# Optimization experiments

Measured on AMD Instinct MI355X. Metric: run time of the kernel, lower is better.

Reference implementation:

```python
import jax, jax.numpy as jnp
import numpy as np

D = 1024  # input_size
H = 1024  # hidden_size
B = 128
R = 512


def _lin(x, W, b):
    return x @ W + b


def setup_inputs() -> dict:
    key = jax.random.key(0)
    ks = jax.random.split(key, 20)
    s = 0.02
    inp = {
        "V": jax.random.normal(ks[0], (B, R, D), jnp.float32),
        "s_t": jax.random.normal(ks[1], (B, D), jnp.float32),
        "h_t": jax.random.normal(ks[2], (B, D), jnp.float32),
        # weights stored [in, out] (y = x @ W + b)
        "Wv": jax.random.normal(ks[3], (D, H), jnp.float32) * s,
        "bv": jnp.zeros((H,), jnp.float32),
        "Wsp": jax.random.normal(ks[4], (D, D), jnp.float32) * s,
        "bsp": jnp.zeros((D,), jnp.float32),
        "Wsa": jax.random.normal(ks[5], (D, H), jnp.float32) * s,
        "bsa": jnp.zeros((H,), jnp.float32),
        "Whp": jax.random.normal(ks[6], (D, D), jnp.float32) * s,
        "bhp": jnp.zeros((D,), jnp.float32),
        "Wha": jax.random.normal(ks[7], (D, H), jnp.float32) * s,
        "bha": jnp.zeros((H,), jnp.float32),
        "Wal": jax.random.normal(ks[8], (H, 1), jnp.float32) * s,
        "bal": jnp.zeros((1,), jnp.float32),
        "Wcp": jax.random.normal(ks[9], (D, D), jnp.float32) * s,
        "bcp": jnp.zeros((D,), jnp.float32),
    }
    return inp


def reference(V, s_t, h_t, Wv, bv, Wsp, bsp, Wsa, bsa, Whp, bhp, Wha, bha, Wal, bal, Wcp, bcp):
    v_embed = jax.nn.relu(_lin(V, Wv, bv))           # [B,R,H]
    s_proj = jax.nn.relu(_lin(s_t, Wsp, bsp))        # [B,D]
    s_att = _lin(s_proj, Wsa, bsa)                   # [B,H]
    h_proj = jnp.tanh(_lin(h_t, Whp, bhp))           # [B,D]
    h_att = _lin(h_proj, Wha, bha)                   # [B,H]
    regions = jnp.concatenate([V, s_proj[:, None, :]], axis=1)           # [B,R+1,D]
    regions_att = jnp.concatenate([v_embed, s_att[:, None, :]], axis=1)  # [B,R+1,H]
    alpha_input = jnp.tanh(regions_att + h_att[:, None, :])              # [B,R+1,H]
    scores = (_lin(alpha_input, Wal, bal)).squeeze(-1)                   # [B,R+1]
    alpha = jax.nn.softmax(scores, axis=1)                               # [B,R+1]
    context = jnp.einsum("br,brd->bd", alpha, regions)                   # [B,D]
    z_t = jnp.tanh(_lin(context + h_proj, Wcp, bcp))                     # [B,D]
    return z_t
```

## Files before the change

### kernel.cpp

```cpp
#include <hip/hip_runtime.h>


typedef __bf16 bf16x8 __attribute__((ext_vector_type(8)));
typedef float floatx4 __attribute__((ext_vector_type(4)));

__device__ __forceinline__ float tanh_fast(float x) {
    x = fminf(10.0f, fmaxf(-10.0f, x));
    float e = exp2f(x * 2.885390081777927f);
    return (e - 1.0f) * __builtin_amdgcn_rcpf(e + 1.0f);
}

__global__ __launch_bounds__(256) void wvt_kernel(
    const float* __restrict__ Wv, __bf16* __restrict__ WvT) {
    __shared__ float tile[64][65];
    const int k0 = blockIdx.x * 64, n0 = blockIdx.y * 64;
    const int c = threadIdx.x & 63, r = threadIdx.x >> 6;
#pragma unroll
    for (int i = 0; i < 16; ++i)
        tile[r + i * 4][c] = Wv[(size_t)(k0 + r + i * 4) * 1024 + n0 + c];
    __syncthreads();
#pragma unroll
    for (int i = 0; i < 16; ++i)
        WvT[(size_t)(n0 + r + i * 4) * 1024 + k0 + c] =
            (__bf16)tile[c][r + i * 4];
}

__global__ __launch_bounds__(512) void small_gemm_k(
    const float* __restrict__ A0, const float* __restrict__ W0,
    const float* __restrict__ b0, float* __restrict__ C0, int act0,
    const float* __restrict__ A1, const float* __restrict__ W1,
    const float* __restrict__ b1, float* __restrict__ C1, int act1) {
    const float* A; const float* W; const float* bs; float* C; int act;
    if (blockIdx.z == 0) { A = A0; W = W0; bs = b0; C = C0; act = act0; }
    else                 { A = A1; W = W1; bs = b1; C = C1; act = act1; }
    __shared__ float red[3][8][128];
    const int tid = threadIdx.x;
    const int nl = tid & 127, kq = tid >> 7;
    const int n = blockIdx.x * 128 + nl;
    const int m0 = blockIdx.y * 8;
    const float* Ab = A + m0 * 1024;
    float acc[8] = {};
    const int kbeg = kq * 256, kend = kbeg + 256;
#pragma unroll 4
    for (int k = kbeg; k < kend; ++k) {
        float w = W[(size_t)k * 1024 + n];
#pragma unroll
        for (int mi = 0; mi < 8; ++mi)
            acc[mi] = fmaf(Ab[mi * 1024 + k], w, acc[mi]);
    }
    if (kq > 0) {
#pragma unroll
        for (int mi = 0; mi < 8; ++mi) red[kq - 1][mi][nl] = acc[mi];
    }
    __syncthreads();
    if (kq == 0) {
        float bias = bs[n];
#pragma unroll
        for (int mi = 0; mi < 8; ++mi) {
            float v = acc[mi] + red[0][mi][nl] + red[1][mi][nl] +
                      red[2][mi][nl] + bias;
            if (act == 1) v = fmaxf(v, 0.0f);
            else if (act == 2) v = tanh_fast(v);
            C[(size_t)(m0 + mi) * 1024 + n] = v;
        }
    }
}

__global__ __launch_bounds__(256, 3) void score_gemm_k(
    const float* __restrict__ V, const __bf16* __restrict__ WvT,
    const float* __restrict__ bv, const float* __restrict__ h_att,
    const float* __restrict__ Wal, float* __restrict__ scores) {
    __shared__ __bf16 As[2][128 * 40];
    __shared__ __bf16 Bs[2][128 * 32];

    const int tid = threadIdx.x;
    const int bid = blockIdx.x;
    const int xcd = bid & 7;
    const int j = bid >> 3;
    const int mtile = xcd * 64 + (j >> 3);
    const int ntile = j & 7;
    const int m0 = mtile * 128, n0 = ntile * 128;
    const int wid = tid >> 6, lane = tid & 63;
    const int wm = wid & 1, wn = wid >> 1;
    const int lcol = lane & 15, quad = lane >> 4;

    floatx4 acc[4][4] = {};

    const int am = tid >> 1;
    const int ak = (tid & 1) * 16;
    const float* aptr = V + (size_t)(m0 + am) * 1024 + ak;

    const int g0n = tid >> 2, g0ks = tid & 3;
    const int g1n = (256 + tid) >> 2, g1ks = tid & 3;
    const int g0kg = g0ks ^ ((g0n >> 1) & 3);
    const int g1kg = g1ks ^ ((g1n >> 1) & 3);
    const __bf16* bp0 = WvT + (size_t)(n0 + g0n) * 1024 + g0kg * 8;
    const __bf16* bp1 = WvT + (size_t)(n0 + g1n) * 1024 + g1kg * 8;

    auto stage_A = [&](int buf, float4 f0, float4 f1, float4 f2, float4 f3) {
        bf16x8 u0, u1;
        u0[0] = (__bf16)f0.x; u0[1] = (__bf16)f0.y;
        u0[2] = (__bf16)f0.z; u0[3] = (__bf16)f0.w;
        u0[4] = (__bf16)f1.x; u0[5] = (__bf16)f1.y;
        u0[6] = (__bf16)f1.z; u0[7] = (__bf16)f1.w;
        u1[0] = (__bf16)f2.x; u1[1] = (__bf16)f2.y;
        u1[2] = (__bf16)f2.z; u1[3] = (__bf16)f2.w;
        u1[4] = (__bf16)f3.x; u1[5] = (__bf16)f3.y;
        u1[6] = (__bf16)f3.z; u1[7] = (__bf16)f3.w;
        __bf16* awr = &As[buf][am * 40 + ak];
        *reinterpret_cast<bf16x8*>(awr) = u0;
        *reinterpret_cast<bf16x8*>(awr + 8) = u1;
    };
    auto dma_B = [&](int buf, int k0) {
        __builtin_amdgcn_global_load_lds(
            (const __attribute__((address_space(1))) void*)(bp0 + k0),
            (__attribute__((address_space(3))) void*)(&Bs[buf][tid * 8]),
            16, 0, 0);
        __builtin_amdgcn_global_load_lds(
            (const __attribute__((address_space(1))) void*)(bp1 + k0),
            (__attribute__((address_space(3))) void*)(&Bs[buf][(256 + tid) * 8]),
            16, 0, 0);
    };

    dma_B(0, 0);
    {
        const float4* fp = reinterpret_cast<const float4*>(aptr);
        stage_A(0, fp[0], fp[1], fp[2], fp[3]);
    }
    __syncthreads();

    for (int kk = 0; kk < 32; ++kk) {
        const int cur = kk & 1, nxt = cur ^ 1;
        float4 f0, f1, f2, f3;
        const bool pf = (kk < 31);
        if (pf) {
            dma_B(nxt, (kk + 1) * 32);
            const float4* fp =
                reinterpret_cast<const float4*>(aptr + (kk + 1) * 32);
            f0 = fp[0]; f1 = fp[1]; f2 = fp[2]; f3 = fp[3];
        }
        bf16x8 af[4], bfr[4];
#pragma unroll
        for (int mi = 0; mi < 4; ++mi)
            af[mi] = *reinterpret_cast<const bf16x8*>(
                &As[cur][(wm * 64 + mi * 16 + lcol) * 40 + quad * 8]);
#pragma unroll
        for (int ni = 0; ni < 4; ++ni) {
            int n = wn * 64 + ni * 16 + lcol;
            int ks = quad ^ ((n >> 1) & 3);
            bfr[ni] = *reinterpret_cast<const bf16x8*>(
                &Bs[cur][n * 32 + ks * 8]);
        }
#pragma unroll
        for (int mi = 0; mi < 4; ++mi)
#pragma unroll
            for (int ni = 0; ni < 4; ++ni)
                acc[mi][ni] = __builtin_amdgcn_mfma_f32_16x16x32_bf16(
                    af[mi], bfr[ni], acc[mi][ni], 0, 0, 0);
        if (pf) stage_A(nxt, f0, f1, f2, f3);
        __syncthreads();
    }

    const int b = m0 >> 9;
    float wal[4], hat[4], bvv[4];
#pragma unroll
    for (int ni = 0; ni < 4; ++ni) {
        int n = n0 + wn * 64 + ni * 16 + lcol;
        wal[ni] = Wal[n];
        hat[ni] = h_att[b * 1024 + n];
        bvv[ni] = bv[n];
    }
    float p[16];
#pragma unroll
    for (int mi = 0; mi < 4; ++mi) {
#pragma unroll
        for (int rg = 0; rg < 4; ++rg) {
            float s = 0.f;
#pragma unroll
            for (int ni = 0; ni < 4; ++ni) {
                float x = acc[mi][ni][rg] + bvv[ni];
                x = fmaxf(x, 0.f);
                s = fmaf(wal[ni], tanh_fast(x + hat[ni]), s);
            }
            p[mi * 4 + rg] = s;
        }
    }
#pragma unroll
    for (int off = 1; off < 16; off <<= 1) {
#pragma unroll
        for (int i = 0; i < 16; ++i) p[i] += __shfl_xor(p[i], off, 64);
    }
    if (lcol == 0) {
#pragma unroll
        for (int mi = 0; mi < 4; ++mi)
#pragma unroll
            for (int rg = 0; rg < 4; ++rg) {
                int row = m0 + wm * 64 + mi * 16 + quad * 4 + rg;
                atomicAdd(&scores[b * 513 + (row & 511)], p[mi * 4 + rg]);
            }
    }
}

__global__ __launch_bounds__(256) void lastrow_k(
    const float* __restrict__ s_att, const float* __restrict__ h_att,
    const float* __restrict__ Wal, float* __restrict__ scores) {
    int b = blockIdx.x, tid = threadIdx.x;
    float s = 0.f;
    for (int h = tid; h < 1024; h += 256)
        s += Wal[h] * tanh_fast(s_att[b * 1024 + h] + h_att[b * 1024 + h]);
#pragma unroll
    for (int off = 32; off >= 1; off >>= 1) s += __shfl_xor(s, off, 64);
    __shared__ float red[4];
    if ((tid & 63) == 0) red[tid >> 6] = s;
    __syncthreads();
    if (tid == 0) scores[b * 513 + 512] = red[0] + red[1] + red[2] + red[3];
}

__global__ __launch_bounds__(256) void softmax_k(
    const float* __restrict__ scores, float* __restrict__ alpha) {
    int b = blockIdx.x, tid = threadIdx.x;
    const float* s = scores + b * 513;
    float v0 = s[tid];
    float v1 = s[tid + 256];
    float v2 = (tid == 0) ? s[512] : -1e30f;
    float m = fmaxf(v0, fmaxf(v1, v2));
#pragma unroll
    for (int off = 32; off >= 1; off >>= 1) m = fmaxf(m, __shfl_xor(m, off, 64));
    __shared__ float red[4];
    int w = tid >> 6;
    if ((tid & 63) == 0) red[w] = m;
    __syncthreads();
    m = fmaxf(fmaxf(red[0], red[1]), fmaxf(red[2], red[3]));
    const float L2E = 1.4426950408889634f;
    float e0 = exp2f((v0 - m) * L2E);
    float e1 = exp2f((v1 - m) * L2E);
    float e2 = (tid == 0) ? exp2f((v2 - m) * L2E) : 0.f;
    float sum = e0 + e1 + e2;
#pragma unroll
    for (int off = 32; off >= 1; off >>= 1) sum += __shfl_xor(sum, off, 64);
    __syncthreads();
    if ((tid & 63) == 0) red[w] = sum;
    __syncthreads();
    sum = red[0] + red[1] + red[2] + red[3];
    float inv = 1.0f / sum;
    float* a = alpha + b * 513;
    a[tid] = e0 * inv;
    a[tid + 256] = e1 * inv;
    if (tid == 0) a[512] = e2 * inv;
}

__global__ __launch_bounds__(256) void ctx_k(
    const float* __restrict__ V, const float* __restrict__ alpha,
    const float* __restrict__ s_proj, const float* __restrict__ h_proj,
    float* __restrict__ ctxsum) {
    const int b = blockIdx.x, dq = blockIdx.y;
    const int tid = threadIdx.x;
    const int dl = tid & 63, rq = tid >> 6;
    __shared__ float sal[513];
    __shared__ float red[3][64][4];
    for (int i = tid; i < 513; i += 256) sal[i] = alpha[b * 513 + i];
    __syncthreads();
    const int d0 = dq * 256 + dl * 4;
    const float* vp = V + ((size_t)b * 512 + rq * 128) * 1024 + d0;
    float a0 = 0, a1 = 0, a2 = 0, a3 = 0;
#pragma unroll 8
    for (int r = 0; r < 128; ++r) {
        float al = sal[rq * 128 + r];
        const float4 vv = *reinterpret_cast<const float4*>(vp + (size_t)r * 1024);
        a0 = fmaf(al, vv.x, a0); a1 = fmaf(al, vv.y, a1);
        a2 = fmaf(al, vv.z, a2); a3 = fmaf(al, vv.w, a3);
    }
    if (rq > 0) {
        red[rq - 1][dl][0] = a0; red[rq - 1][dl][1] = a1;
        red[rq - 1][dl][2] = a2; red[rq - 1][dl][3] = a3;
    }
    __syncthreads();
    if (rq == 0) {
#pragma unroll
        for (int q = 0; q < 3; ++q) {
            a0 += red[q][dl][0]; a1 += red[q][dl][1];
            a2 += red[q][dl][2]; a3 += red[q][dl][3];
        }
        float4 sp = *reinterpret_cast<const float4*>(s_proj + b * 1024 + d0);
        float4 hp = *reinterpret_cast<const float4*>(h_proj + b * 1024 + d0);
        float aR = sal[512];
        float4 o;
        o.x = fmaf(aR, sp.x, a0) + hp.x;
        o.y = fmaf(aR, sp.y, a1) + hp.y;
        o.z = fmaf(aR, sp.z, a2) + hp.z;
        o.w = fmaf(aR, sp.w, a3) + hp.w;
        *reinterpret_cast<float4*>(ctxsum + b * 1024 + d0) = o;
    }
}

extern "C" void kernel_launch(void* const* d_in, const int* in_sizes, int n_in,
                              void* d_out, int out_size, void* d_ws,
                              size_t ws_size, hipStream_t stream) {
    const float* V   = (const float*)d_in[0];
    const float* s_t = (const float*)d_in[1];
    const float* h_t = (const float*)d_in[2];
    const float* Wv  = (const float*)d_in[3];
    const float* bv  = (const float*)d_in[4];
    const float* Wsp = (const float*)d_in[5];
    const float* bsp = (const float*)d_in[6];
    const float* Wsa = (const float*)d_in[7];
    const float* bsa = (const float*)d_in[8];
    const float* Whp = (const float*)d_in[9];
    const float* bhp = (const float*)d_in[10];
    const float* Wha = (const float*)d_in[11];
    const float* bha = (const float*)d_in[12];
    const float* Wal = (const float*)d_in[13];
    const float* Wcp = (const float*)d_in[15];
    const float* bcp = (const float*)d_in[16];
    float* out = (float*)d_out;

    char* ws = (char*)d_ws;
    __bf16* WvT   = (__bf16*)(ws + 0);
    float* s_proj = (float*)(ws + 2097152);
    float* h_proj = (float*)(ws + 2621440);
    float* s_att  = (float*)(ws + 3145728);
    float* h_att  = (float*)(ws + 3670016);
    float* scores = (float*)(ws + 4194304);
    float* alpha  = (float*)(ws + 4456960);
    float* ctxsum = (float*)(ws + 4719616);

    hipLaunchKernelGGL(wvt_kernel, dim3(16, 16), dim3(256), 0, stream, Wv, WvT);
    hipLaunchKernelGGL(small_gemm_k, dim3(8, 16, 2), dim3(512), 0, stream,
                       s_t, Wsp, bsp, s_proj, 1,
                       h_t, Whp, bhp, h_proj, 2);
    hipLaunchKernelGGL(small_gemm_k, dim3(8, 16, 2), dim3(512), 0, stream,
                       s_proj, Wsa, bsa, s_att, 0,
                       h_proj, Wha, bha, h_att, 0);
    (void)hipMemsetAsync(scores, 0, 128 * 513 * sizeof(float), stream);
    hipLaunchKernelGGL(score_gemm_k, dim3(4096), dim3(256), 0, stream,
                       V, WvT, bv, h_att, Wal, scores);
    hipLaunchKernelGGL(lastrow_k, dim3(128), dim3(256), 0, stream,
                       s_att, h_att, Wal, scores);
    hipLaunchKernelGGL(softmax_k, dim3(128), dim3(256), 0, stream,
                       scores, alpha);
    hipLaunchKernelGGL(ctx_k, dim3(128, 4), dim3(256), 0, stream,
                       V, alpha, s_proj, h_proj, ctxsum);
    hipLaunchKernelGGL(small_gemm_k, dim3(8, 16, 1), dim3(512), 0, stream,
                       ctxsum, Wcp, bcp, out, 2,
                       ctxsum, Wcp, bcp, out, 2);
}
```

Before: 892.2 us.

## Pre-convert V to bf16 and stream score GEMM tiles via global_load_lds

Adds a pass that converts V to bf16 in a large workspace buffer. A new score GEMM kernel then loads both operands directly into LDS through async global_load_lds with an XOR swizzle and double buffering. This removes the fp32 load and in-register conversion of V from the GEMM inner loop, and because the old kernel re-reads V for each of the 8 N-tiles, that traffic is also halved. The cost is an extra full read of V plus a write of 128 MB of bf16, and it only runs when the workspace is large enough; otherwise the old kernel is used as a fallback.

```diff
diff --git a/kernel.cpp b/kernel.cpp
--- a/kernel.cpp
+++ b/kernel.cpp
@@ -8,6 +8,19 @@
     x = fminf(10.0f, fmaxf(-10.0f, x));
     float e = exp2f(x * 2.885390081777927f);
     return (e - 1.0f) * __builtin_amdgcn_rcpf(e + 1.0f);
+}
+
+__global__ __launch_bounds__(256) void conv_k(
+    const float* __restrict__ V, __bf16* __restrict__ Vb) {
+    const size_t i = ((size_t)blockIdx.x * 256 + threadIdx.x) * 8;
+    const float4 a = *reinterpret_cast<const float4*>(V + i);
+    const float4 b = *reinterpret_cast<const float4*>(V + i + 4);
+    bf16x8 o;
+    o[0] = (__bf16)a.x; o[1] = (__bf16)a.y;
+    o[2] = (__bf16)a.z; o[3] = (__bf16)a.w;
+    o[4] = (__bf16)b.x; o[5] = (__bf16)b.y;
+    o[6] = (__bf16)b.z; o[7] = (__bf16)b.w;
+    *reinterpret_cast<bf16x8*>(Vb + i) = o;
 }
 
 __global__ __launch_bounds__(256) void wvt_kernel(
@@ -67,6 +80,120 @@
 }
 
 __global__ __launch_bounds__(256, 3) void score_gemm_k(
+    const __bf16* __restrict__ Vb, const __bf16* __restrict__ WvT,
+    const float* __restrict__ bv, const float* __restrict__ h_att,
+    const float* __restrict__ Wal, float* __restrict__ scores) {
+    __shared__ __bf16 As[2][128 * 32];
+    __shared__ __bf16 Bs[2][128 * 32];
+
+    const int tid = threadIdx.x;
+    const int bid = blockIdx.x;
+    const int xcd = bid & 7;
+    const int j = bid >> 3;
+    const int mtile = xcd * 64 + (j >> 3);
+    const int ntile = j & 7;
+    const int m0 = mtile * 128, n0 = ntile * 128;
+    const int wid = tid >> 6, lane = tid & 63;
+    const int wm = wid & 1, wn = wid >> 1;
+    const int lcol = lane & 15, quad = lane >> 4;
+
+    floatx4 acc[4][4] = {};
+
+    const int grow = tid >> 2;
+    const int kg = (tid & 3) ^ ((grow >> 1) & 3);
+    const __bf16* ap0 = Vb + (size_t)(m0 + grow) * 1024 + kg * 8;
+    const __bf16* bp0 = WvT + (size_t)(n0 + grow) * 1024 + kg * 8;
+
+    auto dma = [&](int buf, int k0) {
+        __builtin_amdgcn_global_load_lds(
+            (const __attribute__((address_space(1))) void*)(ap0 + k0),
+            (__attribute__((address_space(3))) void*)(&As[buf][tid * 8]),
+            16, 0, 0);
+        __builtin_amdgcn_global_load_lds(
+            (const __attribute__((address_space(1))) void*)(ap0 + 64 * 1024 + k0),
+            (__attribute__((address_space(3))) void*)(&As[buf][(256 + tid) * 8]),
+            16, 0, 0);
+        __builtin_amdgcn_global_load_lds(
+            (const __attribute__((address_space(1))) void*)(bp0 + k0),
+            (__attribute__((address_space(3))) void*)(&Bs[buf][tid * 8]),
+            16, 0, 0);
+        __builtin_amdgcn_global_load_lds(
+            (const __attribute__((address_space(1))) void*)(bp0 + 64 * 1024 + k0),
+            (__attribute__((address_space(3))) void*)(&Bs[buf][(256 + tid) * 8]),
+            16, 0, 0);
+    };
+
+    dma(0, 0);
+
+    int aoff[4], boff[4];
+#pragma unroll
+    for (int i = 0; i < 4; ++i) {
+        int r = wm * 64 + i * 16 + lcol;
+        aoff[i] = r * 32 + ((quad ^ ((r >> 1) & 3)) * 8);
+        int n = wn * 64 + i * 16 + lcol;
+        boff[i] = n * 32 + ((quad ^ ((n >> 1) & 3)) * 8);
+    }
+    __syncthreads();
+
+    for (int kk = 0; kk < 32; ++kk) {
+        const int cur = kk & 1, nxt = cur ^ 1;
+        if (kk < 31) dma(nxt, (kk + 1) * 32);
+        bf16x8 af[4], bfr[4];
+#pragma unroll
+        for (int i = 0; i < 4; ++i) {
+            af[i] = *reinterpret_cast<const bf16x8*>(&As[cur][aoff[i]]);
+            bfr[i] = *reinterpret_cast<const bf16x8*>(&Bs[cur][boff[i]]);
+        }
+#pragma unroll
+        for (int mi = 0; mi < 4; ++mi)
+#pragma unroll
+            for (int ni = 0; ni < 4; ++ni)
+                acc[mi][ni] = __builtin_amdgcn_mfma_f32_16x16x32_bf16(
+                    af[mi], bfr[ni], acc[mi][ni], 0, 0, 0);
+        __syncthreads();
+    }
+
+    const int b = m0 >> 9;
+    float wal[4], hat[4], bvv[4];
+#pragma unroll
+    for (int ni = 0; ni < 4; ++ni) {
+        int n = n0 + wn * 64 + ni * 16 + lcol;
+        wal[ni] = Wal[n];
+        hat[ni] = h_att[b * 1024 + n];
+        bvv[ni] = bv[n];
+    }
+    float p[16];
+#pragma unroll
+    for (int mi = 0; mi < 4; ++mi) {
+#pragma unroll
+        for (int rg = 0; rg < 4; ++rg) {
+            float s = 0.f;
+#pragma unroll
+            for (int ni = 0; ni < 4; ++ni) {
+                float x = acc[mi][ni][rg] + bvv[ni];
+                x = fmaxf(x, 0.f);
+                s = fmaf(wal[ni], tanh_fast(x + hat[ni]), s);
+            }
+            p[mi * 4 + rg] = s;
+        }
+    }
+#pragma unroll
+    for (int off = 1; off < 16; off <<= 1) {
+#pragma unroll
+        for (int i = 0; i < 16; ++i) p[i] += __shfl_xor(p[i], off, 64);
+    }
+    if (lcol == 0) {
+#pragma unroll
+        for (int mi = 0; mi < 4; ++mi)
+#pragma unroll
+            for (int rg = 0; rg < 4; ++rg) {
+                int row = m0 + wm * 64 + mi * 16 + quad * 4 + rg;
+                atomicAdd(&scores[b * 513 + (row & 511)], p[mi * 4 + rg]);
+            }
+    }
+}
+
+__global__ __launch_bounds__(256, 3) void score_gemm_fb(
     const float* __restrict__ V, const __bf16* __restrict__ WvT,
     const float* __restrict__ bv, const float* __restrict__ h_att,
     const float* __restrict__ Wal, float* __restrict__ scores) {
@@ -314,16 +441,24 @@
     const float* bcp = (const float*)d_in[16];
     float* out = (float*)d_out;
 
+    const size_t VB_BYTES = (size_t)128 * 512 * 1024 * 2;
+    const size_t SMALL_BYTES = 5242880 + 64;
+    const bool big = ws_size >= VB_BYTES + SMALL_BYTES;
+
     char* ws = (char*)d_ws;
-    __bf16* WvT   = (__bf16*)(ws + 0);
-    float* s_proj = (float*)(ws + 2097152);
-    float* h_proj = (float*)(ws + 2621440);
-    float* s_att  = (float*)(ws + 3145728);
-    float* h_att  = (float*)(ws + 3670016);
-    float* scores = (float*)(ws + 4194304);
-    float* alpha  = (float*)(ws + 4456960);
-    float* ctxsum = (float*)(ws + 4719616);
-
+    __bf16* Vb = (__bf16*)ws;
+    char* base = big ? (ws + VB_BYTES) : ws;
+    __bf16* WvT   = (__bf16*)(base + 0);
+    float* s_proj = (float*)(base + 2097152);
+    float* h_proj = (float*)(base + 2621440);
+    float* s_att  = (float*)(base + 3145728);
+    float* h_att  = (float*)(base + 3670016);
+    float* scores = (float*)(base + 4194304);
+    float* alpha  = (float*)(base + 4456960);
+    float* ctxsum = (float*)(base + 4719616);
+
+    if (big)
+        hipLaunchKernelGGL(conv_k, dim3(32768), dim3(256), 0, stream, V, Vb);
     hipLaunchKernelGGL(wvt_kernel, dim3(16, 16), dim3(256), 0, stream, Wv, WvT);
     hipLaunchKernelGGL(small_gemm_k, dim3(8, 16, 2), dim3(512), 0, stream,
                        s_t, Wsp, bsp, s_proj, 1,
@@ -332,8 +467,12 @@
                        s_proj, Wsa, bsa, s_att, 0,
                        h_proj, Wha, bha, h_att, 0);
     (void)hipMemsetAsync(scores, 0, 128 * 513 * sizeof(float), stream);
-    hipLaunchKernelGGL(score_gemm_k, dim3(4096), dim3(256), 0, stream,
-                       V, WvT, bv, h_att, Wal, scores);
+    if (big)
+        hipLaunchKernelGGL(score_gemm_k, dim3(4096), dim3(256), 0, stream,
+                           Vb, WvT, bv, h_att, Wal, scores);
+    else
+        hipLaunchKernelGGL(score_gemm_fb, dim3(4096), dim3(256), 0, stream,
+                           V, WvT, bv, h_att, Wal, scores);
     hipLaunchKernelGGL(lastrow_k, dim3(128), dim3(256), 0, stream,
                        s_att, h_att, Wal, scores);
     hipLaunchKernelGGL(softmax_k, dim3(128), dim3(256), 0, stream,
```

Result: faster. 838.8 us (-6.0%).
